# Kernel tuning notes

Measured on AMD Instinct MI355X. Metric: run time of the kernel, lower is better.

## Reference

```python
import jax, jax.numpy as jnp
import numpy as np

S, B, H, E = 2048, 4, 1024, 8
FF = 4 * H


def openai_gelu(x):
    # Megatron's tanh-approx gelu: 0.5*x*(1+tanh(sqrt(2/pi)*x*(1+0.044715*x^2)))
    return 0.5 * x * (1.0 + jnp.tanh(0.7978845608028654 * x * (1.0 + 0.044715 * x * x)))


def setup_inputs() -> dict:
    key = jax.random.key(0)
    ks = jax.random.split(key, 6)
    hidden_states = jax.random.normal(ks[0], (S, B, H), dtype=jnp.float32)
    # router: nn.Linear(H, E) with bias -> weight [E, H], bias [E]
    router_w = jax.random.normal(ks[1], (E, H), dtype=jnp.float32) / np.sqrt(H)
    router_b = jnp.zeros((E,), dtype=jnp.float32)
    # per-expert MLP weights, stacked on leading expert axis (torch Linear weight = [out, in])
    w1 = jax.random.normal(ks[2], (E, FF, H), dtype=jnp.float32) * np.sqrt(2.0 / (H + FF))
    b1 = jnp.zeros((E, FF), dtype=jnp.float32)
    w2 = jax.random.normal(ks[3], (E, H, FF), dtype=jnp.float32) * np.sqrt(2.0 / (H + FF))
    b2 = jnp.zeros((E, H), dtype=jnp.float32)
    return {"hidden_states": hidden_states, "router_w": router_w, "router_b": router_b,
            "w1": w1, "b1": b1, "w2": w2, "b2": b2}


def reference(hidden_states, router_w, router_b, w1, b1, w2, b2):
    s, b, h = hidden_states.shape
    e = w1.shape[0]
    # router + top-1 selection
    route = jax.nn.softmax(hidden_states @ router_w.T + router_b, axis=2)  # [s,b,E]
    max_prob = jnp.max(route, axis=2).reshape(-1, 1)                       # [N,1]
    max_ind = jnp.argmax(route, axis=2).reshape(-1)                        # [N]
    x = hidden_states.reshape(-1, h)                                       # [N,h]
    out = jnp.zeros_like(x)
    out_bias = jnp.zeros_like(x)
    # E is small and fixed; top-1 routing covers every token exactly once.
    for ei in range(e):
        inter = openai_gelu(x @ w1[ei].T + b1[ei])   # [N, 4h]
        y = inter @ w2[ei].T                          # [N, h]
        mask = (max_ind == ei)[:, None]
        out = jnp.where(mask, y, out)
        out_bias = jnp.where(mask, b2[ei][None, :], out_bias)
    out = (out * max_prob).reshape(s, b, h)
    out_bias = (out_bias * max_prob).reshape(s, b, h)
    return (out, out_bias)
```

## Files before the change

kernel.cpp:

```cpp
#include <hip/hip_runtime.h>
#include <math.h>

typedef float  f32x4  __attribute__((ext_vector_type(4)));
typedef short  bf16x8 __attribute__((ext_vector_type(8)));

#define NTOK 8192
#define H    1024
#define FF   4096
#define NEXP 8
#define MAXTILES 40

__device__ __forceinline__ unsigned short f2bf(float f) {
    unsigned int u = __float_as_uint(f);
    u += 0x7fffu + ((u >> 16) & 1u);
    return (unsigned short)(u >> 16);
}

__device__ __forceinline__ void gload16(const void* g, void* l) {
    __builtin_amdgcn_global_load_lds((const __attribute__((address_space(1))) void*)g,
                                     (__attribute__((address_space(3))) void*)l, 16, 0, 0);
}

__global__ void __launch_bounds__(256)
router_k(const float* __restrict__ x, const float* __restrict__ rw, const float* __restrict__ rb,
         float* __restrict__ maxp, int* __restrict__ maxi, int* __restrict__ counts) {
    const int lane = threadIdx.x & 63;
    const int t = blockIdx.x * 4 + (threadIdx.x >> 6);
    const float4* xr = (const float4*)(x + (size_t)t * H);
    float acc[NEXP];
#pragma unroll
    for (int e = 0; e < NEXP; ++e) acc[e] = 0.f;
#pragma unroll
    for (int c = 0; c < 4; ++c) {
        float4 xv = xr[lane + 64 * c];
#pragma unroll
        for (int e = 0; e < NEXP; ++e) {
            float4 wv = ((const float4*)(rw + e * H))[lane + 64 * c];
            acc[e] += xv.x * wv.x + xv.y * wv.y + xv.z * wv.z + xv.w * wv.w;
        }
    }
#pragma unroll
    for (int e = 0; e < NEXP; ++e) {
#pragma unroll
        for (int off = 32; off > 0; off >>= 1) acc[e] += __shfl_xor(acc[e], off);
    }
    if (lane == 0) {
        float best = -1e30f; int bi = 0;
#pragma unroll
        for (int e = 0; e < NEXP; ++e) {
            float v = acc[e] + rb[e];
            acc[e] = v;
            if (v > best) { best = v; bi = e; }
        }
        float s = 0.f;
#pragma unroll
        for (int e = 0; e < NEXP; ++e) s += __expf(acc[e] - best);
        maxp[t] = 1.0f / s;
        maxi[t] = bi;
        atomicAdd(&counts[bi * 32], 1);
    }
}

__global__ void scan_k(const int* __restrict__ counts, int* __restrict__ offs,
                       int* __restrict__ tile_e, int* __restrict__ tile_r0, int* __restrict__ ntiles) {
    int off = 0, ti = 0;
    for (int e = 0; e < NEXP; ++e) {
        offs[e] = off;
        int c = counts[e * 32];
        int nt = (c + 255) >> 8;
        for (int j = 0; j < nt; ++j) { tile_e[ti] = e; tile_r0[ti] = off + (j << 8); ++ti; }
        off += ((c + 127) >> 7) << 7;
    }
    offs[NEXP] = off;
    *ntiles = ti;
}

__global__ void __launch_bounds__(256)
gather_k(const float* __restrict__ x, const int* __restrict__ maxi, const int* __restrict__ offs,
         int* __restrict__ cursor, int* __restrict__ perm, unsigned short* __restrict__ ab) {
    const int lane = threadIdx.x & 63;
    const int t = blockIdx.x * 4 + (threadIdx.x >> 6);
    int pos = 0;
    if (lane == 0) {
        int e = maxi[t];
        pos = offs[e] + atomicAdd(&cursor[e * 32], 1);
        perm[pos] = t;
    }
    pos = __shfl(pos, 0);
    const float4* xr = (const float4*)(x + (size_t)t * H);
    ushort4* ar = (ushort4*)(ab + (size_t)pos * H);
#pragma unroll
    for (int c = 0; c < 4; ++c) {
        float4 v = xr[lane + 64 * c];
        ar[lane + 64 * c] = make_ushort4(f2bf(v.x), f2bf(v.y), f2bf(v.z), f2bf(v.w));
    }
}

__global__ void __launch_bounds__(256)
cvt_k(const float4* __restrict__ w1, const float4* __restrict__ w2,
      ushort4* __restrict__ d1, ushort4* __restrict__ d2, int n4) {
    const int stride = gridDim.x * blockDim.x;
    for (int i = blockIdx.x * blockDim.x + threadIdx.x; i < n4; i += stride) {
        float4 v = w1[i]; d1[i] = make_ushort4(f2bf(v.x), f2bf(v.y), f2bf(v.z), f2bf(v.w));
        float4 u = w2[i]; d2[i] = make_ushort4(f2bf(u.x), f2bf(u.y), f2bf(u.z), f2bf(u.w));
    }
}


#define READ_A(BA, MH)                                                          \
  _Pragma("unroll") for (int j = 0; j < 4; ++j)                                 \
    _Pragma("unroll") for (int kk = 0; kk < 2; ++kk)                            \
      a_[j][kk] = *(const bf16x8*)((BA) + (wr*8 + (MH)*4 + j)*2048 + kk*1024 + aoffb);

#define READ_B(BB, NH, BR)                                                      \
  _Pragma("unroll") for (int j2 = 0; j2 < 2; ++j2)                              \
    _Pragma("unroll") for (int kk = 0; kk < 2; ++kk)                            \
      BR[j2][kk] = *(const bf16x8*)((BB) + (wc*4 + (NH)*2 + j2)*2048 + kk*1024 + aoffb);

#define MFMA_Q(MH, NH, BR)                                                      \
  __builtin_amdgcn_s_setprio(1);                                                \
  _Pragma("unroll") for (int kk = 0; kk < 2; ++kk)                              \
    _Pragma("unroll") for (int j = 0; j < 4; ++j)                               \
      _Pragma("unroll") for (int j2 = 0; j2 < 2; ++j2)                          \
        asm volatile("v_mfma_f32_16x16x32_bf16 %0, %1, %2, %0"                  \
          : "+v"(acc[(MH)*4 + j][(NH)*2 + j2]) : "v"(a_[j][kk]), "v"(BR[j2][kk])); \
  __builtin_amdgcn_s_setprio(0);

#define BAR() __builtin_amdgcn_s_barrier()

template<int KE>
__device__ __forceinline__ void gemm8_core(const char* __restrict__ Ag, const char* __restrict__ Bg,
                                           char* lds, f32x4 (&acc)[8][4]) {
    constexpr int LD2 = KE * 2;
    const int tid = threadIdx.x, l = tid & 63, w = tid >> 6;
    const int wr = w >> 2, wc = w & 3;
    const int term  = ((l >> 4) * 8) ^ (((l >> 3) & 1) << 4);
    const int aoffb = (l & 15) * 64 + term * 2;

    char* const A0 = lds;          char* const B0 = lds + 32768;
    char* const A1 = lds + 65536;  char* const B1 = lds + 98304;

    int offA[2][2], offB[2][2], dstA[2][2], dstB[2][2];
#pragma unroll
    for (int q = 0; q < 2; ++q) {
        const int s  = q * 8 + w;
        const int lr = l >> 2;
        const int h  = ((s >> 1) << 4) + lr;
        const int c  = ((s & 1) << 5) + (((l & 3) * 8) ^ ((l & 32) >> 1));
#pragma unroll
        for (int half = 0; half < 2; ++half) {
            const int rA = (h & 63) + ((h >> 6) << 7) + (half << 6);
            const int rB = (h & 31) + ((h >> 5) << 6) + (half << 5);
            offA[q][half] = rA * LD2 + c * 2;
            offB[q][half] = rB * LD2 + c * 2;
            dstA[q][half] = ((((s >> 1) & 3) + (half << 2) + ((s >> 3) << 3)) << 11) + ((s & 1) << 10);
            dstB[q][half] = ((((s >> 1) & 1) + (half << 1) + ((s >> 2) << 2)) << 11) + ((s & 1) << 10);
        }
    }
    auto SA = [&](char* dst, int half, int kt) {
        gload16(Ag + offA[0][half] + kt * 128, dst + dstA[0][half]);
        gload16(Ag + offA[1][half] + kt * 128, dst + dstA[1][half]);
    };
    auto SB = [&](char* dst, int half, int kt) {
        gload16(Bg + offB[0][half] + kt * 128, dst + dstB[0][half]);
        gload16(Bg + offB[1][half] + kt * 128, dst + dstB[1][half]);
    };

    SA(A0, 0, 0); SB(B0, 0, 0); SB(B0, 1, 0); SA(A0, 1, 0);
    SA(A1, 0, 1); SB(B1, 0, 1); SB(B1, 1, 1);
    asm volatile("s_waitcnt vmcnt(6)" ::: "memory");
    BAR();

    constexpr int NKT = KE / 64;
    bf16x8 a_[4][2], b0_[2][2], b1_[2][2];
#pragma unroll 1
    for (int k0 = 0; k0 < NKT; k0 += 2) {
        const int k1 = k0 + 1;
        READ_A(A0, 0) READ_B(B0, 0, b0_)
        SA(A1, 1, k1);
        BAR(); MFMA_Q(0, 0, b0_) BAR();
        READ_B(B0, 1, b1_)
        SA(A0, 0, k0 + 2);
        BAR(); MFMA_Q(0, 1, b1_) BAR();
        READ_A(A0, 1)
        SB(B0, 0, k0 + 2);
        BAR(); MFMA_Q(1, 1, b1_) BAR();
        SB(B0, 1, k0 + 2);
        asm volatile("s_waitcnt vmcnt(4)" ::: "memory");
        BAR(); MFMA_Q(1, 0, b0_) BAR();
        READ_A(A1, 0) READ_B(B1, 0, b0_)
        SA(A0, 1, k0 + 2);
        BAR(); MFMA_Q(0, 0, b0_) BAR();
        READ_B(B1, 1, b1_)
        SA(A1, 0, k1 + 2);
        BAR(); MFMA_Q(0, 1, b1_) BAR();
        READ_A(A1, 1)
        SB(B1, 0, k1 + 2);
        BAR(); MFMA_Q(1, 1, b1_) BAR();
        SB(B1, 1, k1 + 2);
        asm volatile("s_waitcnt vmcnt(4)" ::: "memory");
        BAR(); MFMA_Q(1, 0, b0_) BAR();
    }
}

__global__ void __launch_bounds__(512, 2)
gemm1_k(const unsigned short* __restrict__ ab, const unsigned short* __restrict__ w1b,
        const float* __restrict__ b1, unsigned short* __restrict__ inter,
        const int* __restrict__ tile_e, const int* __restrict__ tile_r0,
        const int* __restrict__ ntiles, const int* __restrict__ offs) {
    if ((int)blockIdx.y >= *ntiles) return;
    __shared__ char lds[131072];
    const int e = tile_e[blockIdx.y], row0 = tile_r0[blockIdx.y];
    const int f0 = blockIdx.x * 256;
    f32x4 acc[8][4];
#pragma unroll
    for (int m = 0; m < 8; ++m)
#pragma unroll
        for (int n = 0; n < 4; ++n)
#pragma unroll
            for (int j = 0; j < 4; ++j) acc[m][n][j] = 0.f;

    gemm8_core<H>((const char*)(ab + (size_t)row0 * H),
                  (const char*)(w1b + ((size_t)e * FF + f0) * H), lds, acc);

    const int l = threadIdx.x & 63, w = threadIdx.x >> 6, wr = w >> 2, wc = w & 3;
    const int rend = offs[e + 1];
#pragma unroll
    for (int n = 0; n < 4; ++n) {
        const int col = f0 + wc * 64 + n * 16 + (l & 15);
        const float bias = b1[e * FF + col];
#pragma unroll
        for (int m = 0; m < 8; ++m) {
            const int r0 = row0 + wr * 128 + m * 16 + ((l >> 4) << 2);
#pragma unroll
            for (int j = 0; j < 4; ++j) {
                if (r0 + j < rend) {
                    float v = acc[m][n][j] + bias;
                    float ex = __expf(1.5957691216057308f * v * (1.0f + 0.044715f * v * v));
                    float u  = v - v / (ex + 1.0f);
                    inter[(size_t)(r0 + j) * FF + col] = f2bf(u);
                }
            }
        }
    }
}

__global__ void __launch_bounds__(512, 2)
gemm2_k(const unsigned short* __restrict__ inter, const unsigned short* __restrict__ w2b,
        const float* __restrict__ b2, float* __restrict__ out, float* __restrict__ outb,
        const int* __restrict__ tile_e, const int* __restrict__ tile_r0, const int* __restrict__ ntiles,
        const int* __restrict__ counts, const int* __restrict__ offs,
        const int* __restrict__ perm, const float* __restrict__ maxp) {
    if ((int)blockIdx.y >= *ntiles) return;
    __shared__ char lds[131072];
    const int e = tile_e[blockIdx.y], row0 = tile_r0[blockIdx.y];
    const int h0 = blockIdx.x * 256;
    f32x4 acc[8][4];
#pragma unroll
    for (int m = 0; m < 8; ++m)
#pragma unroll
        for (int n = 0; n < 4; ++n)
#pragma unroll
            for (int j = 0; j < 4; ++j) acc[m][n][j] = 0.f;

    gemm8_core<FF>((const char*)(inter + (size_t)row0 * FF),
                   (const char*)(w2b + ((size_t)e * H + h0) * FF), lds, acc);

    const int l = threadIdx.x & 63, w = threadIdx.x >> 6, wr = w >> 2, wc = w & 3;
    const int cnt = counts[e * 32], offe = offs[e];
#pragma unroll
    for (int m = 0; m < 8; ++m) {
#pragma unroll
        for (int j = 0; j < 4; ++j) {
            const int grow = row0 + wr * 128 + m * 16 + ((l >> 4) << 2) + j;
            if (grow - offe < cnt) {
                const int t = perm[grow];
                const float p = maxp[t];
#pragma unroll
                for (int n = 0; n < 4; ++n) {
                    const int col = h0 + wc * 64 + n * 16 + (l & 15);
                    out [(size_t)t * H + col] = acc[m][n][j] * p;
                    outb[(size_t)t * H + col] = b2[e * H + col] * p;
                }
            }
        }
    }
}

extern "C" void kernel_launch(void* const* d_in, const int* in_sizes, int n_in,
                              void* d_out, int out_size, void* d_ws, size_t ws_size,
                              hipStream_t stream) {
    const float* x  = (const float*)d_in[0];
    const float* rw = (const float*)d_in[1];
    const float* rb = (const float*)d_in[2];
    const float* w1 = (const float*)d_in[3];
    const float* b1 = (const float*)d_in[4];
    const float* w2 = (const float*)d_in[5];
    const float* b2 = (const float*)d_in[6];
    float* out  = (float*)d_out;
    float* outb = out + (size_t)NTOK * H;

    char* ws = (char*)d_ws;
    unsigned short* W1B   = (unsigned short*)(ws);
    unsigned short* W2B   = (unsigned short*)(ws + 67108864);
    unsigned short* AB    = (unsigned short*)(ws + 134217728);
    unsigned short* INTER = (unsigned short*)(ws + 153092096);
    float* MAXP    = (float*)(ws + 228589568);
    int*   MAXI    = (int*)  (ws + 228622336);
    int*   PERM    = (int*)  (ws + 228655104);
    int*   COUNTS  = (int*)  (ws + 228691968);
    int*   CURSOR  = (int*)  (ws + 228692992);
    int*   OFFS    = (int*)  (ws + 228694016);
    int*   TILE_E  = (int*)  (ws + 228694080);
    int*   TILE_R0 = (int*)  (ws + 228694336);
    int*   NTILES  = (int*)  (ws + 228694592);

    (void)hipMemsetAsync(COUNTS, 0, 2048, stream);

    router_k<<<NTOK / 4, 256, 0, stream>>>(x, rw, rb, MAXP, MAXI, COUNTS);
    scan_k<<<1, 1, 0, stream>>>(COUNTS, OFFS, TILE_E, TILE_R0, NTILES);
    gather_k<<<NTOK / 4, 256, 0, stream>>>(x, MAXI, OFFS, CURSOR, PERM, AB);
    cvt_k<<<4096, 256, 0, stream>>>((const float4*)w1, (const float4*)w2,
                                    (ushort4*)W1B, (ushort4*)W2B, NEXP * FF * H / 4);
    gemm1_k<<<dim3(FF / 256, MAXTILES), 512, 0, stream>>>(AB, W1B, b1, INTER,
                                                          TILE_E, TILE_R0, NTILES, OFFS);
    gemm2_k<<<dim3(H / 256, MAXTILES), 512, 0, stream>>>(INTER, W2B, b2, out, outb,
                                                         TILE_E, TILE_R0, NTILES,
                                                         COUNTS, OFFS, PERM, MAXP);
}
```

Before: 400.6 us.

## Split-K gemm2 with atomics, LDS-staged gemm1 epilogue, XCD-aware block remap

Gemm2 now splits the K dimension in two, doubling the block count, and accumulates into a zeroed output with atomic adds. Gemm1's epilogue goes through a swizzled LDS tile so the bf16 intermediate is written with coalesced 16-byte stores. Both GEMMs use a 1D grid remapped so neighbouring work lands on the same XCD, and the MFMA accumulators are constrained to AGPRs. In exchange there is an extra memset of the output, atomic traffic, and a possible change in register pressure.

```diff
diff --git a/kernel.cpp b/kernel.cpp
--- a/kernel.cpp
+++ b/kernel.cpp
@@ -3,6 +3,7 @@
 
 typedef float  f32x4  __attribute__((ext_vector_type(4)));
 typedef short  bf16x8 __attribute__((ext_vector_type(8)));
+typedef unsigned short ushort8 __attribute__((ext_vector_type(8)));
 
 #define NTOK 8192
 #define H    1024
@@ -123,15 +124,15 @@
     _Pragma("unroll") for (int j = 0; j < 4; ++j)                               \
       _Pragma("unroll") for (int j2 = 0; j2 < 2; ++j2)                          \
         asm volatile("v_mfma_f32_16x16x32_bf16 %0, %1, %2, %0"                  \
-          : "+v"(acc[(MH)*4 + j][(NH)*2 + j2]) : "v"(a_[j][kk]), "v"(BR[j2][kk])); \
+          : "+a"(acc[(MH)*4 + j][(NH)*2 + j2]) : "v"(a_[j][kk]), "v"(BR[j2][kk])); \
   __builtin_amdgcn_s_setprio(0);
 
 #define BAR() __builtin_amdgcn_s_barrier()
 
-template<int KE>
+template<int KE, int LDE>
 __device__ __forceinline__ void gemm8_core(const char* __restrict__ Ag, const char* __restrict__ Bg,
                                            char* lds, f32x4 (&acc)[8][4]) {
-    constexpr int LD2 = KE * 2;
+    constexpr int LD2 = LDE * 2;
     const int tid = threadIdx.x, l = tid & 63, w = tid >> 6;
     const int wr = w >> 2, wc = w & 3;
     const int term  = ((l >> 4) * 8) ^ (((l >> 3) & 1) << 4);
@@ -208,10 +209,13 @@
         const float* __restrict__ b1, unsigned short* __restrict__ inter,
         const int* __restrict__ tile_e, const int* __restrict__ tile_r0,
         const int* __restrict__ ntiles, const int* __restrict__ offs) {
-    if ((int)blockIdx.y >= *ntiles) return;
+    const int bid = blockIdx.x;
+    const int wkid = (bid & 7) * 80 + (bid >> 3);
+    const int xb = wkid / MAXTILES, yb = wkid % MAXTILES;
+    if (yb >= *ntiles) return;
     __shared__ char lds[131072];
-    const int e = tile_e[blockIdx.y], row0 = tile_r0[blockIdx.y];
-    const int f0 = blockIdx.x * 256;
+    const int e = tile_e[yb], row0 = tile_r0[yb];
+    const int f0 = xb * 256;
     f32x4 acc[8][4];
 #pragma unroll
     for (int m = 0; m < 8; ++m)
@@ -220,27 +224,41 @@
 #pragma unroll
             for (int j = 0; j < 4; ++j) acc[m][n][j] = 0.f;
 
-    gemm8_core<H>((const char*)(ab + (size_t)row0 * H),
-                  (const char*)(w1b + ((size_t)e * FF + f0) * H), lds, acc);
-
-    const int l = threadIdx.x & 63, w = threadIdx.x >> 6, wr = w >> 2, wc = w & 3;
+    gemm8_core<H, H>((const char*)(ab + (size_t)row0 * H),
+                     (const char*)(w1b + ((size_t)e * FF + f0) * H), lds, acc);
+
+    asm volatile("s_waitcnt vmcnt(0)" ::: "memory");
+    __syncthreads();
+    const int tid = threadIdx.x, l = tid & 63, w = tid >> 6, wr = w >> 2, wc = w & 3;
+    const int q = (l >> 4) & 3, lc = l & 15;
+    unsigned short* cl = (unsigned short*)lds;
+    float bias[4];
+#pragma unroll
+    for (int n = 0; n < 4; ++n) bias[n] = b1[e * FF + f0 + wc * 64 + n * 16 + lc];
+    const int rowb = wr * 128 + q * 4;
+#pragma unroll
+    for (int n = 0; n < 4; ++n) {
+        const int coln = (wc * 64 + n * 16 + lc) ^ (q << 4);
+#pragma unroll
+        for (int m = 0; m < 8; ++m)
+#pragma unroll
+            for (int j = 0; j < 4; ++j) {
+                float v = acc[m][n][j] + bias[n];
+                float ex = __expf(1.5957691216057308f * v * (1.0f + 0.044715f * v * v));
+                float u  = v - v / (ex + 1.0f);
+                cl[(rowb + m * 16 + j) * 256 + coln] = f2bf(u);
+            }
+    }
+    __syncthreads();
     const int rend = offs[e + 1];
-#pragma unroll
-    for (int n = 0; n < 4; ++n) {
-        const int col = f0 + wc * 64 + n * 16 + (l & 15);
-        const float bias = b1[e * FF + col];
-#pragma unroll
-        for (int m = 0; m < 8; ++m) {
-            const int r0 = row0 + wr * 128 + m * 16 + ((l >> 4) << 2);
-#pragma unroll
-            for (int j = 0; j < 4; ++j) {
-                if (r0 + j < rend) {
-                    float v = acc[m][n][j] + bias;
-                    float ex = __expf(1.5957691216057308f * v * (1.0f + 0.044715f * v * v));
-                    float u  = v - v / (ex + 1.0f);
-                    inter[(size_t)(r0 + j) * FF + col] = f2bf(u);
-                }
-            }
+    const int rsub = tid >> 5, cblk = (tid & 31) * 8;
+    const int rxor = ((rsub >> 2) & 3) << 4;
+#pragma unroll
+    for (int it = 0; it < 16; ++it) {
+        const int r = it * 16 + rsub;
+        if (row0 + r < rend) {
+            ushort8 val = *(const ushort8*)&cl[r * 256 + (cblk ^ rxor)];
+            *(ushort8*)&inter[(size_t)(row0 + r) * FF + f0 + cblk] = val;
         }
     }
 }
@@ -251,10 +269,14 @@
         const int* __restrict__ tile_e, const int* __restrict__ tile_r0, const int* __restrict__ ntiles,
         const int* __restrict__ counts, const int* __restrict__ offs,
         const int* __restrict__ perm, const float* __restrict__ maxp) {
-    if ((int)blockIdx.y >= *ntiles) return;
+    const int bid = blockIdx.x;
+    const int wkid = (bid & 7) * 40 + (bid >> 3);
+    const int combo = wkid / MAXTILES, yb = wkid % MAXTILES;
+    const int xb = combo >> 1, sp = combo & 1;
+    if (yb >= *ntiles) return;
     __shared__ char lds[131072];
-    const int e = tile_e[blockIdx.y], row0 = tile_r0[blockIdx.y];
-    const int h0 = blockIdx.x * 256;
+    const int e = tile_e[yb], row0 = tile_r0[yb];
+    const int h0 = xb * 256;
     f32x4 acc[8][4];
 #pragma unroll
     for (int m = 0; m < 8; ++m)
@@ -263,8 +285,8 @@
 #pragma unroll
             for (int j = 0; j < 4; ++j) acc[m][n][j] = 0.f;
 
-    gemm8_core<FF>((const char*)(inter + (size_t)row0 * FF),
-                   (const char*)(w2b + ((size_t)e * H + h0) * FF), lds, acc);
+    gemm8_core<2048, FF>((const char*)(inter + (size_t)row0 * FF + sp * 2048),
+                         (const char*)(w2b + ((size_t)e * H + h0) * FF + sp * 2048), lds, acc);
 
     const int l = threadIdx.x & 63, w = threadIdx.x >> 6, wr = w >> 2, wc = w & 3;
     const int cnt = counts[e * 32], offe = offs[e];
@@ -279,8 +301,8 @@
 #pragma unroll
                 for (int n = 0; n < 4; ++n) {
                     const int col = h0 + wc * 64 + n * 16 + (l & 15);
-                    out [(size_t)t * H + col] = acc[m][n][j] * p;
-                    outb[(size_t)t * H + col] = b2[e * H + col] * p;
+                    unsafeAtomicAdd(&out[(size_t)t * H + col], acc[m][n][j] * p);
+                    if (sp == 0) outb[(size_t)t * H + col] = b2[e * H + col] * p;
                 }
             }
         }
@@ -316,15 +338,16 @@
     int*   NTILES  = (int*)  (ws + 228694592);
 
     (void)hipMemsetAsync(COUNTS, 0, 2048, stream);
+    (void)hipMemsetAsync(out, 0, (size_t)NTOK * H * 4, stream);
 
     router_k<<<NTOK / 4, 256, 0, stream>>>(x, rw, rb, MAXP, MAXI, COUNTS);
     scan_k<<<1, 1, 0, stream>>>(COUNTS, OFFS, TILE_E, TILE_R0, NTILES);
     gather_k<<<NTOK / 4, 256, 0, stream>>>(x, MAXI, OFFS, CURSOR, PERM, AB);
     cvt_k<<<4096, 256, 0, stream>>>((const float4*)w1, (const float4*)w2,
                                     (ushort4*)W1B, (ushort4*)W2B, NEXP * FF * H / 4);
-    gemm1_k<<<dim3(FF / 256, MAXTILES), 512, 0, stream>>>(AB, W1B, b1, INTER,
-                                                          TILE_E, TILE_R0, NTILES, OFFS);
-    gemm2_k<<<dim3(H / 256, MAXTILES), 512, 0, stream>>>(INTER, W2B, b2, out, outb,
-                                                         TILE_E, TILE_R0, NTILES,
-                                                         COUNTS, OFFS, PERM, MAXP);
-}
+    gemm1_k<<<16 * MAXTILES, 512, 0, stream>>>(AB, W1B, b1, INTER,
+                                               TILE_E, TILE_R0, NTILES, OFFS);
+    gemm2_k<<<8 * MAXTILES, 512, 0, stream>>>(INTER, W2B, b2, out, outb,
+                                              TILE_E, TILE_R0, NTILES,
+                                              COUNTS, OFFS, PERM, MAXP);
+}
```

Result: slower. 723.1 us (+80.5%).
